# Performance work log

Hardware: AMD Instinct MI355X
Metric: run time of the kernel (lower is better)

## Reference

```python
import jax, jax.numpy as jnp
import numpy as np

N = 100000      # nodes
E = 800000      # edges (nnz of sparse adj)
D_IN = 128      # input feature dim
H = 64          # hidden_units
EMB = 32        # embsize
N_IDX = 50000   # gathered output rows
EPS = 1e-05     # BatchNormalization epsilon


def spmm(rows, cols, vals, x):
    # out[i] = sum_{e: rows[e]==i} vals[e] * x[cols[e]]  == sparse A @ x
    return jax.ops.segment_sum(vals[:, None] * x[cols], rows, num_segments=N)


def batchnorm(x, gamma, beta):
    # training-mode BN over node (batch) axis, matching Keras BatchNormalization
    m = jnp.mean(x, axis=0)
    v = jnp.var(x, axis=0)
    return (x - m) * jax.lax.rsqrt(v + EPS) * gamma + beta


def setup_inputs() -> dict:
    key = jax.random.key(0)
    ks = jax.random.split(key, 16)
    def w(k, fan_in, shape):
        return jax.random.normal(k, shape, dtype=jnp.float32) / np.sqrt(fan_in)
    inp = {
        "features": jax.random.normal(ks[0], (N, D_IN), dtype=jnp.float32),
        "rows": jax.random.randint(ks[1], (E,), 0, N),
        "cols": jax.random.randint(ks[2], (E,), 0, N),
        "vals": jax.random.uniform(ks[3], (E,), dtype=jnp.float32),
        "idx": jax.random.randint(ks[4], (N_IDX,), 0, N),
        # layer 0 (Dense with bias since l==0)
        "Wn0": w(ks[5], D_IN, (D_IN, H)), "bn0": jnp.zeros((H,), jnp.float32),
        "Wg0": w(ks[6], D_IN, (D_IN, H)), "bg0": jnp.zeros((H,), jnp.float32),
        "ab0": jnp.zeros((H,), jnp.float32),  # BiasLayer after SpMM
        "g0": jnp.ones((H,), jnp.float32), "b0": jnp.zeros((H,), jnp.float32),
        # layer 1 (no Dense bias)
        "Wn1": w(ks[7], H, (H, H)),
        "Wg1": w(ks[8], H, (H, H)),
        "ab1": jnp.zeros((H,), jnp.float32),
        "g1": jnp.ones((H,), jnp.float32), "b1": jnp.zeros((H,), jnp.float32),
        # conv_last block (Dense use_bias=False)
        "WnL": w(ks[9], H, (H, EMB)),
        "WgL": w(ks[10], H, (H, EMB)),
        "abL": jnp.zeros((EMB,), jnp.float32),
    }
    return inp


def reference(features, rows, cols, vals, idx,
              Wn0, bn0, Wg0, bg0, ab0, g0, b0,
              Wn1, Wg1, ab1, g1, b1,
              WnL, WgL, abL):
    x = features
    # SAGE layer 0
    x_node = x @ Wn0 + bn0
    x_neigh = x @ Wg0 + bg0
    agg = spmm(rows, cols, vals, x_neigh) + ab0
    x = jax.nn.relu(batchnorm(x_node + agg, g0, b0))
    # SAGE layer 1
    x_node = x @ Wn1
    x_neigh = x @ Wg1
    agg = spmm(rows, cols, vals, x_neigh) + ab1
    x = jax.nn.relu(batchnorm(x_node + agg, g1, b1))
    # conv_last projection to embsize
    x_node = x @ WnL
    x_neigh = x @ WgL
    agg = spmm(rows, cols, vals, x_neigh) + abL
    x = x_node + agg
    return x[idx]
```

## Files before the change

### kernel.cpp

```cpp
#include <hip/hip_runtime.h>

#define NNODES 100000
#define NEDGES 800000
#define DIN    128
#define HID    64
#define EMB    32
#define NIDX   50000
#define BN_EPS 1e-5f

#define NCHK 64
#define EC   (NEDGES / NCHK)
#define NB   ((NNODES + 63) / 64)
#define PF   16
#define NBF  ((NB + PF - 1) / PF)

typedef __attribute__((ext_vector_type(8))) short short8;
typedef __attribute__((ext_vector_type(4))) float f32x4;

__device__ inline unsigned short f2bf(float f) {
    unsigned u = __float_as_uint(f);
    unsigned r = u + 0x7FFFu + ((u >> 16) & 1u);
    return (unsigned short)(r >> 16);
}
__device__ inline float bf2f_lo(unsigned u) { return __uint_as_float(u << 16); }
__device__ inline float bf2f_hi(unsigned u) { return __uint_as_float(u & 0xffff0000u); }


__device__ inline void pack_seg(const float* __restrict__ Wn, const float* __restrict__ Wg,
                                unsigned short* __restrict__ Wp, int HOUT, int l2nt, int f) {
    int j = f & 7, lane = (f >> 3) & 63, g = f >> 9;
    int tt = g & ((1 << l2nt) - 1), kb = g >> l2nt;
    int k = kb * 32 + ((lane >> 4) * 8) + j;
    int nn = tt * 16 + (lane & 15);
    float v = (nn < HOUT) ? Wn[k * HOUT + nn] : Wg[k * HOUT + (nn - HOUT)];
    Wp[f] = f2bf(v);
}


__global__ __launch_bounds__(256) void histpack_k(
    const int* __restrict__ rows, int* __restrict__ Bcnt4, int* __restrict__ bTot,
    const int* __restrict__ idx, int* __restrict__ mark,
    const float* Wn0, const float* Wg0, const float* Wn1,
    const float* Wg1, const float* WnL, const float* WgL,
    unsigned short* Wp0, unsigned short* Wp1, unsigned short* WpL, int MB)
{
    int blk = blockIdx.x;
    int t = threadIdx.x;
    if (blk >= NCHK + MB) {
        int f = (blk - NCHK - MB) * 256 + t;
        if (f < 16384)      pack_seg(Wn0, Wg0, Wp0, 64, 3, f);
        else if (f < 24576) pack_seg(Wn1, Wg1, Wp1, 64, 3, f - 16384);
        else if (f < 28672) pack_seg(WnL, WgL, WpL, 32, 2, f - 24576);
        return;
    }
    if (blk >= NCHK) {
        int j = (blk - NCHK) * 256 + t;
        if (j < NIDX) mark[idx[j]] = 1;
        return;
    }
    __shared__ int hist[NB];
    for (int b = t; b < NB; b += 256) hist[b] = 0;
    __syncthreads();
    const int* rbase = rows + blk * EC;
    for (int i4 = t; i4 < EC / 4; i4 += 256) {
        int4 r4 = *(const int4*)&rbase[i4 * 4];
        atomicAdd(&hist[r4.x >> 6], 1);
        atomicAdd(&hist[r4.y >> 6], 1);
        atomicAdd(&hist[r4.z >> 6], 1);
        atomicAdd(&hist[r4.w >> 6], 1);
    }
    __syncthreads();
    for (int b = t; b < NB; b += 256) {
        int h = hist[b];
        Bcnt4[blk * NB + b] = h;
        if (h) atomicAdd(&bTot[b], h);
    }
}

__global__ __launch_bounds__(256) void scan_k(
    const int* __restrict__ Bcnt4, int* __restrict__ BcntT,
    const int* __restrict__ bTot, int* __restrict__ bBase)
{
    int t = threadIdx.x;
    if (blockIdx.x < 7) {
        int b = blockIdx.x * 256 + t;
        if (b >= NB) return;
        int run = 0;
        for (int c = 0; c < NCHK; c++) {
            BcntT[c * NB + b] = run;
            run += Bcnt4[c * NB + b];
        }
        return;
    }
    __shared__ int s[256];
    int v[7], loc = 0;
#pragma unroll
    for (int i = 0; i < 7; i++) {
        int ix = t * 7 + i;
        v[i] = loc;
        loc += (ix < NB) ? bTot[ix] : 0;
    }
    s[t] = loc;
    __syncthreads();
    for (int off = 1; off < 256; off <<= 1) {
        int a = (t >= off) ? s[t - off] : 0;
        __syncthreads();
        s[t] += a;
        __syncthreads();
    }
    int base = s[t] - loc;
#pragma unroll
    for (int i = 0; i < 7; i++) {
        int ix = t * 7 + i;
        if (ix < NB) bBase[ix] = base + v[i];
    }
    if (t == 255) bBase[NB] = NEDGES;
}


__global__ __launch_bounds__(256) void bfinal_spmm0_k(
    const uint2* __restrict__ ebuf, const int* __restrict__ bBase,
    int* __restrict__ rowptr, int2* __restrict__ cs,
    const unsigned short* __restrict__ Hgb, unsigned short* __restrict__ S,
    float* __restrict__ stats, int n)
{
    constexpr int ECAP = 1024;
    __shared__ int hist[64], sc[64], cur[64];
    __shared__ int2 es2[ECAP];
    __shared__ float rs[16][HID], rq[16][HID];
    int b = blockIdx.x, t = threadIdx.x;
    int e0 = bBase[b], e1 = bBase[b + 1];
    int cnt = e1 - e0;
    int r0 = b << 6;
    if (t < 64) hist[t] = 0;
    __syncthreads();

    uint2 ev0, ev1, ev2, ev3;
    bool h0 = t < cnt, h1 = t + 256 < cnt, h2 = t + 512 < cnt, h3 = t + 768 < cnt;
    if (h0) { ev0 = ebuf[e0 + t];       atomicAdd(&hist[(ev0.x >> 20) & 63], 1); }
    if (h1) { ev1 = ebuf[e0 + t + 256]; atomicAdd(&hist[(ev1.x >> 20) & 63], 1); }
    if (h2) { ev2 = ebuf[e0 + t + 512]; atomicAdd(&hist[(ev2.x >> 20) & 63], 1); }
    if (h3) { ev3 = ebuf[e0 + t + 768]; atomicAdd(&hist[(ev3.x >> 20) & 63], 1); }
    for (int i = t + ECAP; i < cnt; i += 256) {
        uint2 v = ebuf[e0 + i];
        atomicAdd(&hist[(v.x >> 20) & 63], 1);
    }
    __syncthreads();
    if (t == 0) {
        int run = 0;
        for (int j = 0; j < 64; j++) { sc[j] = run; run += hist[j]; }
    }
    __syncthreads();
    if (t < 64) {
        cur[t] = sc[t];
        int r = r0 + t;
        if (r < NNODES) rowptr[r] = e0 + sc[t];
    }
    if (b == NB - 1 && t == 0) rowptr[NNODES] = NEDGES;
    __syncthreads();

#define SCAT(V)                                                          \
    {                                                                    \
        int p = atomicAdd(&cur[((V).x >> 20) & 63], 1);                  \
        int2 pay = make_int2((int)((V).x & 0xFFFFF), (int)(V).y);        \
        if (p < ECAP) es2[p] = pay; else cs[e0 + p] = pay;               \
    }
    if (h0) SCAT(ev0)
    if (h1) SCAT(ev1)
    if (h2) SCAT(ev2)
    if (h3) SCAT(ev3)
    for (int i = t + ECAP; i < cnt; i += 256) {
        uint2 v = ebuf[e0 + i];
        SCAT(v)
    }
#undef SCAT
    __syncthreads();

    int scnt = min(cnt, ECAP);
    for (int i = t; i < scnt; i += 256) cs[e0 + i] = es2[i];

    const int lane = t & 15, g = t >> 4;
    const int c0 = lane * 4;
    float4 sum = make_float4(0.f, 0.f, 0.f, 0.f);
    float4 sq  = make_float4(0.f, 0.f, 0.f, 0.f);
#define FE(i) ((i) < ECAP ? es2[(i)] : cs[e0 + (i)])
#pragma unroll
    for (int rr = 0; rr < 4; rr++) {
        int lr = g * 4 + rr;
        int row = r0 + lr;
        if (row >= n) break;
        int le0 = sc[lr], le1 = sc[lr] + hist[lr];
        uint2 h = *(const uint2*)&S[(size_t)row * HID + c0];
        float4 a0 = make_float4(bf2f_lo(h.x), bf2f_hi(h.x), bf2f_lo(h.y), bf2f_hi(h.y));
        float4 a1 = make_float4(0.f, 0.f, 0.f, 0.f), a2 = a1, a3 = a1;
        int e = le0;
        for (; e + 3 < le1; e += 4) {
            int2 p0 = FE(e), p1 = FE(e + 1), p2 = FE(e + 2), p3 = FE(e + 3);
            float v0 = __int_as_float(p0.y), v1 = __int_as_float(p1.y);
            float v2 = __int_as_float(p2.y), v3 = __int_as_float(p3.y);
            uint2 h0v = *(const uint2*)&Hgb[(size_t)p0.x * HID + c0];
            uint2 h1v = *(const uint2*)&Hgb[(size_t)p1.x * HID + c0];
            uint2 h2v = *(const uint2*)&Hgb[(size_t)p2.x * HID + c0];
            uint2 h3v = *(const uint2*)&Hgb[(size_t)p3.x * HID + c0];
            a0.x += v0 * bf2f_lo(h0v.x); a0.y += v0 * bf2f_hi(h0v.x);
            a0.z += v0 * bf2f_lo(h0v.y); a0.w += v0 * bf2f_hi(h0v.y);
            a1.x += v1 * bf2f_lo(h1v.x); a1.y += v1 * bf2f_hi(h1v.x);
            a1.z += v1 * bf2f_lo(h1v.y); a1.w += v1 * bf2f_hi(h1v.y);
            a2.x += v2 * bf2f_lo(h2v.x); a2.y += v2 * bf2f_hi(h2v.x);
            a2.z += v2 * bf2f_lo(h2v.y); a2.w += v2 * bf2f_hi(h2v.y);
            a3.x += v3 * bf2f_lo(h3v.x); a3.y += v3 * bf2f_hi(h3v.x);
            a3.z += v3 * bf2f_lo(h3v.y); a3.w += v3 * bf2f_hi(h3v.y);
        }
        for (; e < le1; e++) {
            int2 p = FE(e);
            float v = __int_as_float(p.y);
            uint2 hh = *(const uint2*)&Hgb[(size_t)p.x * HID + c0];
            a0.x += v * bf2f_lo(hh.x); a0.y += v * bf2f_hi(hh.x);
            a0.z += v * bf2f_lo(hh.y); a0.w += v * bf2f_hi(hh.y);
        }
        float4 acc = make_float4(a0.x + a1.x + a2.x + a3.x, a0.y + a1.y + a2.y + a3.y,
                                 a0.z + a1.z + a2.z + a3.z, a0.w + a1.w + a2.w + a3.w);
        uint2 o;
        o.x = (unsigned)f2bf(acc.x) | ((unsigned)f2bf(acc.y) << 16);
        o.y = (unsigned)f2bf(acc.z) | ((unsigned)f2bf(acc.w) << 16);
        *(uint2*)&S[(size_t)row * HID + c0] = o;
        sum.x += acc.x; sum.y += acc.y; sum.z += acc.z; sum.w += acc.w;
        sq.x += acc.x * acc.x; sq.y += acc.y * acc.y;
        sq.z += acc.z * acc.z; sq.w += acc.w * acc.w;
    }
#undef FE

    *(float4*)&rs[g][c0] = sum;
    *(float4*)&rq[g][c0] = sq;
    __syncthreads();
    if (t < HID) {
        float a = 0.f, bb = 0.f;
        for (int w = 0; w < 16; w++) { a += rs[w][t]; bb += rq[w][t]; }
        int stripe = b & 7;
        atomicAdd(&stats[stripe * 128 + t], a);
        atomicAdd(&stats[stripe * 128 + HID + t], bb);
    }
}


template <int K, int HOUT, bool AFF, bool XBF, bool HNBF>
__device__ void gemm_body(const void* __restrict__ Xv, const unsigned short* __restrict__ Wp,
                          const float* __restrict__ bnA, const float* __restrict__ bnB,
                          const float* __restrict__ bgA,
                          const float* __restrict__ sums, const float* __restrict__ gamma,
                          const float* __restrict__ beta,
                          float* __restrict__ Hnf, unsigned short* __restrict__ Hnb,
                          unsigned short* __restrict__ Hgb, int n, int blk)
{
    constexpr int NT = 2 * HOUT / 16, NKB = K / 32;
    constexpr int RS = K + 8;
    constexpr int OC = HNBF ? 2 * HOUT : HOUT;
    constexpr int RSE = OC + 8;
    constexpr int XSZ = (RS > RSE) ? RS : RSE;
    __shared__ unsigned short Xs[64 * XSZ];
    __shared__ float sSc[64], sSh[64];

    const int row0 = blk * 64;
    const int t = threadIdx.x;

    if (AFF) {
        if (t < 64) {
            float sum = 0.f, sq = 0.f;
#pragma unroll
            for (int s = 0; s < 8; s++) { sum += sums[s * 128 + t]; sq += sums[s * 128 + 64 + t]; }
            float m = sum / (float)NNODES;
            float var = sq / (float)NNODES - m * m;
            float sc = gamma[t] * rsqrtf(var + BN_EPS);
            sSc[t] = sc; sSh[t] = beta[t] - m * sc;
        }
        __syncthreads();
    }

    constexpr int SIT = K / 32;
    if constexpr (XBF) {
        uint4 u[SIT];
#pragma unroll
        for (int it = 0; it < SIT; it++) {
            int li = it * 256 + t;
            int rr = row0 + li / (K / 8);
            int k8 = (li % (K / 8)) * 8;
            int rc = rr < n ? rr : n - 1;
            u[it] = *(const uint4*)((const unsigned short*)Xv + (size_t)rc * K + k8);
        }
#pragma unroll
        for (int it = 0; it < SIT; it++) {
            int li = it * 256 + t;
            int r  = li / (K / 8);
            int k8 = (li % (K / 8)) * 8;
            float v[8];
            v[0] = bf2f_lo(u[it].x); v[1] = bf2f_hi(u[it].x);
            v[2] = bf2f_lo(u[it].y); v[3] = bf2f_hi(u[it].y);
            v[4] = bf2f_lo(u[it].z); v[5] = bf2f_hi(u[it].z);
            v[6] = bf2f_lo(u[it].w); v[7] = bf2f_hi(u[it].w);
            if (AFF) {
#pragma unroll
                for (int i = 0; i < 8; i++) v[i] = fmaxf(v[i] * sSc[k8 + i] + sSh[k8 + i], 0.f);
            }
            uint4 o;
            o.x = (unsigned)f2bf(v[0]) | ((unsigned)f2bf(v[1]) << 16);
            o.y = (unsigned)f2bf(v[2]) | ((unsigned)f2bf(v[3]) << 16);
            o.z = (unsigned)f2bf(v[4]) | ((unsigned)f2bf(v[5]) << 16);
            o.w = (unsigned)f2bf(v[6]) | ((unsigned)f2bf(v[7]) << 16);
            *(uint4*)&Xs[r * RS + k8] = o;
        }
    } else {
        const float* Xf = (const float*)Xv;
        float4 a[SIT], b[SIT];
#pragma unroll
        for (int it = 0; it < SIT; it++) {
            int li = it * 256 + t;
            int rr = row0 + li / (K / 8);
            int k8 = (li % (K / 8)) * 8;
            int rc = rr < n ? rr : n - 1;
            a[it] = *(const float4*)&Xf[(size_t)rc * K + k8];
            b[it] = *(const float4*)&Xf[(size_t)rc * K + k8 + 4];
        }
#pragma unroll
        for (int it = 0; it < SIT; it++) {
            int li = it * 256 + t;
            int r  = li / (K / 8);
            int k8 = (li % (K / 8)) * 8;
            float v[8] = { a[it].x, a[it].y, a[it].z, a[it].w,
                           b[it].x, b[it].y, b[it].z, b[it].w };
            if (AFF) {
#pragma unroll
                for (int i = 0; i < 8; i++) v[i] = fmaxf(v[i] * sSc[k8 + i] + sSh[k8 + i], 0.f);
            }
            uint4 o;
            o.x = (unsigned)f2bf(v[0]) | ((unsigned)f2bf(v[1]) << 16);
            o.y = (unsigned)f2bf(v[2]) | ((unsigned)f2bf(v[3]) << 16);
            o.z = (unsigned)f2bf(v[4]) | ((unsigned)f2bf(v[5]) << 16);
            o.w = (unsigned)f2bf(v[6]) | ((unsigned)f2bf(v[7]) << 16);
            *(uint4*)&Xs[r * RS + k8] = o;
        }
    }
    __syncthreads();

    const int wave = t >> 6, lane = t & 63;
    const int q = lane >> 4, mrow = lane & 15;

    f32x4 acc[NT];
#pragma unroll
    for (int i = 0; i < NT; i++) acc[i] = (f32x4){0.f, 0.f, 0.f, 0.f};

    const short8* wp8 = (const short8*)Wp;
#pragma unroll
    for (int kb = 0; kb < NKB; kb++) {
        short8 va = *(const short8*)&Xs[(wave * 16 + mrow) * RS + kb * 32 + q * 8];
#pragma unroll
        for (int tt = 0; tt < NT; tt++) {
            short8 vb = wp8[(kb * NT + tt) * 64 + lane];
            acc[tt] = __builtin_amdgcn_mfma_f32_16x16x32_bf16(va, vb, acc[tt], 0, 0, 0);
        }
    }

    __syncthreads();
#pragma unroll
    for (int tt = 0; tt < NT; tt++) {
        int nglob = tt * 16 + mrow;
        bool nside = (nglob < HOUT);
        int c = nside ? nglob : (nglob - HOUT);
        float bias = 0.f;
        if (nside) {
            if (bnA) bias += bnA[c];
            if (bnB) bias += bnB[c];
        } else if (bgA) {
            bias += bgA[c];
        }
        if (HNBF || !nside) {
            int cc = HNBF ? nglob : c;
#pragma unroll
            for (int r = 0; r < 4; r++)
                Xs[(wave * 16 + q * 4 + r) * RSE + cc] = f2bf(acc[tt][r] + bias);
        } else {
#pragma unroll
            for (int r = 0; r < 4; r++) {
                int rr = row0 + wave * 16 + q * 4 + r;
                if (rr < n) Hnf[(size_t)rr * HOUT + c] = acc[tt][r] + bias;
            }
        }
    }
    __syncthreads();
    constexpr int J = OC / 8;
#pragma unroll
    for (int u2 = 0; u2 < (64 * J) / 256; u2++) {
        int li = u2 * 256 + t;
        int r = li / J, j = li % J;
        int rr = row0 + r;
        if (rr < n) {
            uint4 v = *(const uint4*)&Xs[r * RSE + j * 8];
            int c8 = j * 8;
            if (HNBF && c8 < HOUT)
                *(uint4*)&Hnb[(size_t)rr * HOUT + c8] = v;
            else
                *(uint4*)&Hgb[(size_t)rr * HOUT + (HNBF ? c8 - HOUT : c8)] = v;
        }
    }
}

__global__ __launch_bounds__(256) void part_gemm0_k(
    const int* __restrict__ rows, const int* __restrict__ cols,
    const float* __restrict__ vals, const int* __restrict__ BcntT,
    const int* __restrict__ bBase, uint2* __restrict__ ebuf,
    const float* __restrict__ X, const unsigned short* __restrict__ Wp0,
    const float* __restrict__ bn0, const float* __restrict__ ab0, const float* __restrict__ bg0,
    unsigned short* __restrict__ Hn0b, unsigned short* __restrict__ Hgb, int n)
{
    if ((int)blockIdx.x < NCHK * PF) {
        __shared__ int cur[NBF];
        int t = threadIdx.x;
        int blk = blockIdx.x % NCHK;
        int pf  = blockIdx.x / NCHK;
        int b0 = pf * NBF, b1 = (pf == PF - 1) ? NB : (b0 + NBF);
        for (int b = b0 + t; b < b1; b += 256)
            cur[b - b0] = bBase[b] + BcntT[blk * NB + b];
        __syncthreads();
        constexpr int EC4 = EC / 4;
        const int*   rbase = rows + blk * EC;
        const int*   cbase = cols + blk * EC;
        const float* vbase = vals + blk * EC;
        int i4 = t;
        int4 r4, c4; float4 v4;
        if (i4 < EC4) {
            r4 = *(const int4*)&rbase[i4 * 4];
            c4 = *(const int4*)&cbase[i4 * 4];
            v4 = *(const float4*)&vbase[i4 * 4];
        }
        while (i4 < EC4) {
            int4 rr = r4; int4 cc = c4; float4 vv = v4;
            int ni = i4 + 256;
            if (ni < EC4) {
                r4 = *(const int4*)&rbase[ni * 4];
                c4 = *(const int4*)&cbase[ni * 4];
                v4 = *(const float4*)&vbase[ni * 4];
            }
#pragma unroll
            for (int j = 0; j < 4; j++) {
                int r = (&rr.x)[j];
                int b = r >> 6;
                if (b >= b0 && b < b1) {
                    int p = atomicAdd(&cur[b - b0], 1);
                    ebuf[p] = make_uint2(((unsigned)(r & 63) << 20) | (unsigned)(&cc.x)[j],
                                         (unsigned)__float_as_int((&vv.x)[j]));
                }
            }
            i4 = ni;
        }
    } else {
        gemm_body<DIN, HID, false, false, true>(X, Wp0, bn0, ab0, bg0,
            nullptr, nullptr, nullptr, nullptr, Hn0b, Hgb, n, blockIdx.x - NCHK * PF);
    }
}

template <int K, int HOUT, bool AFF, bool XBF, bool HNBF>
__global__ __launch_bounds__(256) void gemm_k(
    const void* __restrict__ X, const unsigned short* __restrict__ Wp,
    const float* __restrict__ bnA, const float* __restrict__ bnB, const float* __restrict__ bgA,
    const float* __restrict__ sums, const float* __restrict__ gamma, const float* __restrict__ beta,
    float* __restrict__ Hnf, unsigned short* __restrict__ Hnb, unsigned short* __restrict__ Hgb, int n)
{
    gemm_body<K, HOUT, AFF, XBF, HNBF>(X, Wp, bnA, bnB, bgA, sums, gamma, beta,
                                       Hnf, Hnb, Hgb, n, blockIdx.x);
}


template <int HH, bool STATS, bool SBF, bool MARKED>
__global__ __launch_bounds__(256) void spmm_k(
    const int* __restrict__ rowptr, const int2* __restrict__ cs,
    const unsigned short* __restrict__ Hgb, void* __restrict__ Sv,
    float* __restrict__ stats, const int* __restrict__ mark, int n)
{
    constexpr int L   = HH / 4;
    constexpr int GP  = 256 / L;
    constexpr int RPB = 64;
    constexpr int RPG = RPB / GP;
    constexpr int ECAP = 1024;
    __shared__ int2 es[ECAP];
    __shared__ int  rp[RPB + 1];

    const int t = threadIdx.x;
    const int R0 = blockIdx.x * RPB;
    if (t <= RPB) rp[t] = rowptr[min(R0 + t, n)];
    __syncthreads();
    const int e0b  = rp[0];
    const int scnt = min(rp[RPB] - e0b, ECAP);
    for (int i = t; i < scnt; i += 256) es[i] = cs[e0b + i];
    __syncthreads();

    const int lane = t % L;
    const int g    = t / L;
    const int c0   = lane * 4;

    float4 sum = make_float4(0.f, 0.f, 0.f, 0.f);
    float4 sq  = make_float4(0.f, 0.f, 0.f, 0.f);

#define SPMM_ROW(FETCH)                                                            \
    {                                                                              \
        int e = le0;                                                               \
        for (; e + 3 < le1; e += 4) {                                              \
            int2 p0 = FETCH(e), p1 = FETCH(e + 1), p2 = FETCH(e + 2), p3 = FETCH(e + 3); \
            float v0 = __int_as_float(p0.y), v1 = __int_as_float(p1.y);            \
            float v2 = __int_as_float(p2.y), v3 = __int_as_float(p3.y);            \
            uint2 h0 = *(const uint2*)&Hgb[(size_t)p0.x * HH + c0];                \
            uint2 h1 = *(const uint2*)&Hgb[(size_t)p1.x * HH + c0];                \
            uint2 h2 = *(const uint2*)&Hgb[(size_t)p2.x * HH + c0];                \
            uint2 h3 = *(const uint2*)&Hgb[(size_t)p3.x * HH + c0];                \
            a0.x += v0 * bf2f_lo(h0.x); a0.y += v0 * bf2f_hi(h0.x);                \
            a0.z += v0 * bf2f_lo(h0.y); a0.w += v0 * bf2f_hi(h0.y);                \
            a1.x += v1 * bf2f_lo(h1.x); a1.y += v1 * bf2f_hi(h1.x);                \
            a1.z += v1 * bf2f_lo(h1.y); a1.w += v1 * bf2f_hi(h1.y);                \
            a2.x += v2 * bf2f_lo(h2.x); a2.y += v2 * bf2f_hi(h2.x);                \
            a2.z += v2 * bf2f_lo(h2.y); a2.w += v2 * bf2f_hi(h2.y);                \
            a3.x += v3 * bf2f_lo(h3.x); a3.y += v3 * bf2f_hi(h3.x);                \
            a3.z += v3 * bf2f_lo(h3.y); a3.w += v3 * bf2f_hi(h3.y);                \
        }                                                                          \
        for (; e < le1; e++) {                                                     \
            int2 p = FETCH(e);                                                     \
            float v = __int_as_float(p.y);                                         \
            uint2 h = *(const uint2*)&Hgb[(size_t)p.x * HH + c0];                  \
            a0.x += v * bf2f_lo(h.x); a0.y += v * bf2f_hi(h.x);                    \
            a0.z += v * bf2f_lo(h.y); a0.w += v * bf2f_hi(h.y);                    \
        }                                                                          \
    }
#define F_LDS(i) es[(i)]
#define F_GLB(i) cs[e0b + (i)]

#pragma unroll
    for (int rr = 0; rr < RPG; rr++) {
        int row = R0 + g * RPG + rr;
        if (row >= n) break;
        if (MARKED && !mark[row]) continue;
        int le0 = rp[g * RPG + rr] - e0b;
        int le1 = rp[g * RPG + rr + 1] - e0b;
        float4 a0, a1, a2, a3;
        if (SBF) {
            uint2 h = *(const uint2*)((const unsigned short*)Sv + (size_t)row * HH + c0);
            a0 = make_float4(bf2f_lo(h.x), bf2f_hi(h.x), bf2f_lo(h.y), bf2f_hi(h.y));
        } else {
            a0 = *(const float4*)((const float*)Sv + (size_t)row * HH + c0);
        }
        a1 = a2 = a3 = make_float4(0.f, 0.f, 0.f, 0.f);
        if (le1 <= scnt) SPMM_ROW(F_LDS) else SPMM_ROW(F_GLB);
        float4 acc = make_float4(a0.x + a1.x + a2.x + a3.x, a0.y + a1.y + a2.y + a3.y,
                                 a0.z + a1.z + a2.z + a3.z, a0.w + a1.w + a2.w + a3.w);
        if (SBF) {
            uint2 o;
            o.x = (unsigned)f2bf(acc.x) | ((unsigned)f2bf(acc.y) << 16);
            o.y = (unsigned)f2bf(acc.z) | ((unsigned)f2bf(acc.w) << 16);
            *(uint2*)((unsigned short*)Sv + (size_t)row * HH + c0) = o;
        } else {
            *(float4*)((float*)Sv + (size_t)row * HH + c0) = acc;
        }
        if (STATS) {
            sum.x += acc.x; sum.y += acc.y; sum.z += acc.z; sum.w += acc.w;
            sq.x += acc.x * acc.x; sq.y += acc.y * acc.y;
            sq.z += acc.z * acc.z; sq.w += acc.w * acc.w;
        }
    }
#undef SPMM_ROW
#undef F_LDS
#undef F_GLB

    if constexpr (STATS) {
        __shared__ float rs[GP][HH];
        __shared__ float rq[GP][HH];
        *(float4*)&rs[g][c0] = sum;
        *(float4*)&rq[g][c0] = sq;
        __syncthreads();
        if (threadIdx.x < HH) {
            float a = 0.f, b = 0.f;
            for (int w = 0; w < GP; w++) { a += rs[w][threadIdx.x]; b += rq[w][threadIdx.x]; }
            int stripe = blockIdx.x & 7;
            atomicAdd(&stats[stripe * 128 + threadIdx.x], a);
            atomicAdd(&stats[stripe * 128 + HH + threadIdx.x], b);
        }
    }
}

__global__ void gather_k(const float* __restrict__ S, const int* __restrict__ idx,
                         float* __restrict__ out, int total4) {
    int j = blockIdx.x * 256 + threadIdx.x;
    if (j < total4) {
        int r = j / (EMB / 4), c4 = (j % (EMB / 4)) * 4;
        *(float4*)&out[(size_t)j * 4] = *(const float4*)&S[(size_t)idx[r] * EMB + c4];
    }
}


extern "C" void kernel_launch(void* const* d_in, const int* in_sizes, int n_in,
                              void* d_out, int out_size, void* d_ws, size_t ws_size,
                              hipStream_t stream) {
    const float* features = (const float*)d_in[0];
    const int*   rows     = (const int*)d_in[1];
    const int*   cols     = (const int*)d_in[2];
    const float* vals     = (const float*)d_in[3];
    const int*   idx      = (const int*)d_in[4];
    const float* Wn0 = (const float*)d_in[5];
    const float* bn0 = (const float*)d_in[6];
    const float* Wg0 = (const float*)d_in[7];
    const float* bg0 = (const float*)d_in[8];
    const float* ab0 = (const float*)d_in[9];
    const float* g0  = (const float*)d_in[10];
    const float* b0  = (const float*)d_in[11];
    const float* Wn1 = (const float*)d_in[12];
    const float* Wg1 = (const float*)d_in[13];
    const float* ab1 = (const float*)d_in[14];
    const float* g1  = (const float*)d_in[15];
    const float* b1  = (const float*)d_in[16];
    const float* WnL = (const float*)d_in[17];
    const float* WgL = (const float*)d_in[18];
    const float* abL = (const float*)d_in[19];
    float* out = (float*)d_out;

    float*          HnLf = (float*)d_ws;
    unsigned short* nA   = (unsigned short*)(HnLf + (size_t)NNODES * EMB);
    unsigned short* nB   = nA + (size_t)NNODES * HID;
    unsigned short* Hgb  = nB + (size_t)NNODES * HID;
    uint2* ebuf  = (uint2*)(Hgb + (size_t)NNODES * HID);
    int2*  cs    = (int2*)(ebuf + NEDGES);
    int*   rowptr = (int*)(cs + NEDGES);
    int*   Bcnt4 = rowptr + (NNODES + 4);
    int*   BcntT = Bcnt4 + NCHK * NB;
    int*   bBase = BcntT + NCHK * NB;
    unsigned short* Wp0 = (unsigned short*)(bBase + 1568);
    unsigned short* Wp1 = Wp0 + 16384;
    unsigned short* WpL = Wp1 + 8192;
    float* stats = (float*)(WpL + 4096);
    int*   mark  = (int*)(stats + 2304);
    int*   bTot  = mark + NNODES;
    float* sums0 = stats;
    float* sums1 = stats + 1024;
    size_t zbytes = 2304 * 4 + (size_t)NNODES * 4 + 1568 * 4;

    hipMemsetAsync(stats, 0, zbytes, stream);

    const int GBm = (NNODES + 63) / 64;
    const int MB  = (NIDX + 255) / 256;

    histpack_k<<<NCHK + MB + 112, 256, 0, stream>>>(
        rows, Bcnt4, bTot, idx, mark, Wn0, Wg0, Wn1, Wg1, WnL, WgL, Wp0, Wp1, WpL, MB);
    scan_k<<<8, 256, 0, stream>>>(Bcnt4, BcntT, bTot, bBase);
    part_gemm0_k<<<NCHK * PF + GBm, 256, 0, stream>>>(rows, cols, vals, BcntT, bBase, ebuf,
                                                      features, Wp0, bn0, ab0, bg0,
                                                      nA, Hgb, NNODES);
    bfinal_spmm0_k<<<NB, 256, 0, stream>>>(ebuf, bBase, rowptr, cs, Hgb, nA, sums0, NNODES);

    gemm_k<HID, HID, true, true, true><<<GBm, 256, 0, stream>>>(
        nA, Wp1, ab1, nullptr, nullptr, sums0, g0, b0, nullptr, nB, Hgb, NNODES);
    spmm_k<HID, true, true, false><<<GBm, 256, 0, stream>>>(rowptr, cs, Hgb, nB, sums1, nullptr, NNODES);

    gemm_k<HID, EMB, true, true, false><<<GBm, 256, 0, stream>>>(
        nB, WpL, abL, nullptr, nullptr, sums1, g1, b1, HnLf, nullptr, Hgb, NNODES);
    spmm_k<EMB, false, false, true><<<GBm, 256, 0, stream>>>(rowptr, cs, Hgb, HnLf, nullptr, mark, NNODES);

    gather_k<<<(NIDX * EMB / 4 + 255) / 256, 256, 0, stream>>>(HnLf, idx, out, NIDX * EMB / 4);
}
```

Baseline: 252.4 us.

## Fuse tail GEMM/SpMM/gather launches into one cooperative kernel with grid syncs

Replaces the five tail launches (layer-1 GEMM, SpMM with stats, last GEMM, marked SpMM, gather) with a single cooperative kernel that separates the phases with grid.sync(). Shared memory is unified into one byte buffer so every phase fits the same occupancy budget. The goal is to remove launch gaps and the ramp-up and drain between dependent kernels. In exchange it adds grid-wide barrier cost and caps occupancy at 7 blocks per CU. The old launch path remains as a fallback when cooperative launch is unsupported or fails.

```diff
diff --git a/kernel.cpp b/kernel.cpp
--- a/kernel.cpp
+++ b/kernel.cpp
@@ -1,4 +1,7 @@
 #include <hip/hip_runtime.h>
+#include <hip/hip_cooperative_groups.h>
+
+namespace cg = cooperative_groups;
 
 #define NNODES 100000
 #define NEDGES 800000
@@ -13,6 +16,8 @@
 #define NB   ((NNODES + 63) / 64)
 #define PF   16
 #define NBF  ((NB + PF - 1) / PF)
+#define GBM  ((NNODES + 63) / 64)
+#define SMSZ 17920
 
 typedef __attribute__((ext_vector_type(8))) short short8;
 typedef __attribute__((ext_vector_type(4))) float f32x4;
@@ -250,15 +255,17 @@
                           const float* __restrict__ sums, const float* __restrict__ gamma,
                           const float* __restrict__ beta,
                           float* __restrict__ Hnf, unsigned short* __restrict__ Hnb,
-                          unsigned short* __restrict__ Hgb, int n, int blk)
+                          unsigned short* __restrict__ Hgb, int n, int blk, char* sm)
 {
     constexpr int NT = 2 * HOUT / 16, NKB = K / 32;
     constexpr int RS = K + 8;
     constexpr int OC = HNBF ? 2 * HOUT : HOUT;
     constexpr int RSE = OC + 8;
     constexpr int XSZ = (RS > RSE) ? RS : RSE;
-    __shared__ unsigned short Xs[64 * XSZ];
-    __shared__ float sSc[64], sSh[64];
+    static_assert(64 * XSZ * 2 + 512 <= SMSZ, "smem budget");
+    unsigned short* Xs = (unsigned short*)sm;
+    float* sSc = (float*)(sm + 64 * XSZ * 2);
+    float* sSh = sSc + 64;
 
     const int row0 = blk * 64;
     const int t = threadIdx.x;
@@ -411,8 +418,9 @@
     const float* __restrict__ bn0, const float* __restrict__ ab0, const float* __restrict__ bg0,
     unsigned short* __restrict__ Hn0b, unsigned short* __restrict__ Hgb, int n)
 {
+    __shared__ alignas(16) char sm[SMSZ];
     if ((int)blockIdx.x < NCHK * PF) {
-        __shared__ int cur[NBF];
+        int* cur = (int*)sm;
         int t = threadIdx.x;
         int blk = blockIdx.x % NCHK;
         int pf  = blockIdx.x / NCHK;
@@ -453,7 +461,7 @@
         }
     } else {
         gemm_body<DIN, HID, false, false, true>(X, Wp0, bn0, ab0, bg0,
-            nullptr, nullptr, nullptr, nullptr, Hn0b, Hgb, n, blockIdx.x - NCHK * PF);
+            nullptr, nullptr, nullptr, nullptr, Hn0b, Hgb, n, blockIdx.x - NCHK * PF, sm);
     }
 }
 
@@ -464,27 +472,31 @@
     const float* __restrict__ sums, const float* __restrict__ gamma, const float* __restrict__ beta,
     float* __restrict__ Hnf, unsigned short* __restrict__ Hnb, unsigned short* __restrict__ Hgb, int n)
 {
+    __shared__ alignas(16) char sm[SMSZ];
     gemm_body<K, HOUT, AFF, XBF, HNBF>(X, Wp, bnA, bnB, bgA, sums, gamma, beta,
-                                       Hnf, Hnb, Hgb, n, blockIdx.x);
+                                       Hnf, Hnb, Hgb, n, blockIdx.x, sm);
 }
 
 
 template <int HH, bool STATS, bool SBF, bool MARKED>
-__global__ __launch_bounds__(256) void spmm_k(
+__device__ void spmm_phase(
     const int* __restrict__ rowptr, const int2* __restrict__ cs,
     const unsigned short* __restrict__ Hgb, void* __restrict__ Sv,
-    float* __restrict__ stats, const int* __restrict__ mark, int n)
+    float* __restrict__ stats, const int* __restrict__ mark, int n, int blk, char* sm)
 {
     constexpr int L   = HH / 4;
     constexpr int GP  = 256 / L;
     constexpr int RPB = 64;
     constexpr int RPG = RPB / GP;
     constexpr int ECAP = 1024;
-    __shared__ int2 es[ECAP];
-    __shared__ int  rp[RPB + 1];
+    static_assert(8464 + 2 * GP * HH * 4 <= SMSZ, "smem budget");
+    int2*  es  = (int2*)sm;
+    int*   rp  = (int*)(sm + 8192);
+    float* rsb = (float*)(sm + 8464);
+    float* rqb = rsb + GP * HH;
 
     const int t = threadIdx.x;
-    const int R0 = blockIdx.x * RPB;
+    const int R0 = blk * RPB;
     if (t <= RPB) rp[t] = rowptr[min(R0 + t, n)];
     __syncthreads();
     const int e0b  = rp[0];
@@ -567,19 +579,27 @@
 #undef F_GLB
 
     if constexpr (STATS) {
-        __shared__ float rs[GP][HH];
-        __shared__ float rq[GP][HH];
-        *(float4*)&rs[g][c0] = sum;
-        *(float4*)&rq[g][c0] = sq;
+        *(float4*)&rsb[g * HH + c0] = sum;
+        *(float4*)&rqb[g * HH + c0] = sq;
         __syncthreads();
-        if (threadIdx.x < HH) {
+        if (t < HH) {
             float a = 0.f, b = 0.f;
-            for (int w = 0; w < GP; w++) { a += rs[w][threadIdx.x]; b += rq[w][threadIdx.x]; }
-            int stripe = blockIdx.x & 7;
-            atomicAdd(&stats[stripe * 128 + threadIdx.x], a);
-            atomicAdd(&stats[stripe * 128 + HH + threadIdx.x], b);
-        }
-    }
+            for (int w = 0; w < GP; w++) { a += rsb[w * HH + t]; b += rqb[w * HH + t]; }
+            int stripe = blk & 7;
+            atomicAdd(&stats[stripe * 128 + t], a);
+            atomicAdd(&stats[stripe * 128 + HH + t], b);
+        }
+    }
+}
+
+template <int HH, bool STATS, bool SBF, bool MARKED>
+__global__ __launch_bounds__(256) void spmm_k(
+    const int* __restrict__ rowptr, const int2* __restrict__ cs,
+    const unsigned short* __restrict__ Hgb, void* __restrict__ Sv,
+    float* __restrict__ stats, const int* __restrict__ mark, int n)
+{
+    __shared__ alignas(16) char sm[SMSZ];
+    spmm_phase<HH, STATS, SBF, MARKED>(rowptr, cs, Hgb, Sv, stats, mark, n, blockIdx.x, sm);
 }
 
 __global__ void gather_k(const float* __restrict__ S, const int* __restrict__ idx,
@@ -588,6 +608,37 @@
     if (j < total4) {
         int r = j / (EMB / 4), c4 = (j % (EMB / 4)) * 4;
         *(float4*)&out[(size_t)j * 4] = *(const float4*)&S[(size_t)idx[r] * EMB + c4];
+    }
+}
+
+
+__global__ __launch_bounds__(256, 7) void tail_k(
+    const unsigned short* nA, const unsigned short* Wp1, const float* ab1,
+    const float* sums0, const float* g0, const float* b0,
+    unsigned short* nB, unsigned short* Hgb,
+    const int* rowptr, const int2* cs, float* sums1,
+    const unsigned short* WpL, const float* abL, const float* g1, const float* b1,
+    float* HnLf, const int* mark, const int* idx, float* out, int n)
+{
+    __shared__ alignas(16) char sm[SMSZ];
+    const int blk = blockIdx.x;
+    cg::grid_group grid = cg::this_grid();
+
+    gemm_body<HID, HID, true, true, true>(nA, Wp1, ab1, nullptr, nullptr,
+        sums0, g0, b0, nullptr, nB, Hgb, n, blk, sm);
+    grid.sync();
+    spmm_phase<HID, true, true, false>(rowptr, cs, Hgb, nB, sums1, nullptr, n, blk, sm);
+    grid.sync();
+    gemm_body<HID, EMB, true, true, false>(nB, WpL, abL, nullptr, nullptr,
+        sums1, g1, b1, HnLf, nullptr, Hgb, n, blk, sm);
+    grid.sync();
+    spmm_phase<EMB, false, false, true>(rowptr, cs, Hgb, HnLf, nullptr, mark, n, blk, sm);
+    grid.sync();
+    int j = blk * 256 + threadIdx.x;
+    constexpr int total4 = NIDX * EMB / 4;
+    if (j < total4) {
+        int r = j / (EMB / 4), c4 = (j % (EMB / 4)) * 4;
+        *(float4*)&out[(size_t)j * 4] = *(const float4*)&HnLf[(size_t)idx[r] * EMB + c4];
     }
 }
 
@@ -639,7 +690,7 @@
 
     hipMemsetAsync(stats, 0, zbytes, stream);
 
-    const int GBm = (NNODES + 63) / 64;
+    const int GBm = GBM;
     const int MB  = (NIDX + 255) / 256;
 
     histpack_k<<<NCHK + MB + 112, 256, 0, stream>>>(
@@ -650,13 +701,33 @@
                                                       nA, Hgb, NNODES);
     bfinal_spmm0_k<<<NB, 256, 0, stream>>>(ebuf, bBase, rowptr, cs, Hgb, nA, sums0, NNODES);
 
-    gemm_k<HID, HID, true, true, true><<<GBm, 256, 0, stream>>>(
-        nA, Wp1, ab1, nullptr, nullptr, sums0, g0, b0, nullptr, nB, Hgb, NNODES);
-    spmm_k<HID, true, true, false><<<GBm, 256, 0, stream>>>(rowptr, cs, Hgb, nB, sums1, nullptr, NNODES);
-
-    gemm_k<HID, EMB, true, true, false><<<GBm, 256, 0, stream>>>(
-        nB, WpL, abL, nullptr, nullptr, sums1, g1, b1, HnLf, nullptr, Hgb, NNODES);
-    spmm_k<EMB, false, false, true><<<GBm, 256, 0, stream>>>(rowptr, cs, Hgb, HnLf, nullptr, mark, NNODES);
-
-    gather_k<<<(NIDX * EMB / 4 + 255) / 256, 256, 0, stream>>>(HnLf, idx, out, NIDX * EMB / 4);
-}
+    static int coop_ok = -1;
+    if (coop_ok < 0) {
+        int dev = 0, sup = 0, ncu = 0, mb = 0;
+        hipGetDevice(&dev);
+        hipDeviceGetAttribute(&sup, hipDeviceAttributeCooperativeLaunch, dev);
+        hipDeviceGetAttribute(&ncu, hipDeviceAttributeMultiprocessorCount, dev);
+        hipOccupancyMaxActiveBlocksPerMultiprocessor(&mb, tail_k, 256, 0);
+        coop_ok = (sup && (long)mb * ncu >= GBM) ? 1 : 0;
+    }
+    if (coop_ok == 1) {
+        int nn = NNODES;
+        void* ka[] = { (void*)&nA, (void*)&Wp1, (void*)&ab1, (void*)&sums0,
+                       (void*)&g0, (void*)&b0, (void*)&nB, (void*)&Hgb,
+                       (void*)&rowptr, (void*)&cs, (void*)&sums1, (void*)&WpL,
+                       (void*)&abL, (void*)&g1, (void*)&b1, (void*)&HnLf,
+                       (void*)&mark, (void*)&idx, (void*)&out, (void*)&nn };
+        hipError_t e = hipLaunchCooperativeKernel((const void*)tail_k, dim3(GBm), dim3(256),
+                                                  ka, 0, stream);
+        if (e != hipSuccess) coop_ok = 0;
+    }
+    if (coop_ok != 1) {
+        gemm_k<HID, HID, true, true, true><<<GBm, 256, 0, stream>>>(
+            nA, Wp1, ab1, nullptr, nullptr, sums0, g0, b0, nullptr, nB, Hgb, NNODES);
+        spmm_k<HID, true, true, false><<<GBm, 256, 0, stream>>>(rowptr, cs, Hgb, nB, sums1, nullptr, NNODES);
+        gemm_k<HID, EMB, true, true, false><<<GBm, 256, 0, stream>>>(
+            nB, WpL, abL, nullptr, nullptr, sums1, g1, b1, HnLf, nullptr, Hgb, NNODES);
+        spmm_k<EMB, false, false, true><<<GBm, 256, 0, stream>>>(rowptr, cs, Hgb, HnLf, nullptr, mark, NNODES);
+        gather_k<<<(NIDX * EMB / 4 + 255) / 256, 256, 0, stream>>>(HnLf, idx, out, NIDX * EMB / 4);
+    }
+}
```

Measured after the change: 274.0 us. 1.09x slower.

## Fold bucket scan into histogram kernel via last-block completion counter

Applied to the files above, without the earlier changes.

Removes the separate scan kernel launch. The last histogram block to finish, detected with an atomic done counter and thread fences, computes the exclusive scan of bucket totals into bBase. The per-chunk prefix (BcntT) is no longer materialized; each partition block in part_gemm0_k instead sums Bcnt4 over earlier chunks on the fly. This trades one kernel launch and a transposed scan for redundant per-block prefix loops of up to 64 loads per bucket, and adds a serialized tail in the last histogram block.

```diff
diff --git a/kernel.cpp b/kernel.cpp
--- a/kernel.cpp
+++ b/kernel.cpp
@@ -39,6 +39,7 @@
 
 __global__ __launch_bounds__(256) void histpack_k(
     const int* __restrict__ rows, int* __restrict__ Bcnt4, int* __restrict__ bTot,
+    int* __restrict__ done, int* __restrict__ bBase,
     const int* __restrict__ idx, int* __restrict__ mark,
     const float* Wn0, const float* Wg0, const float* Wn1,
     const float* Wg1, const float* WnL, const float* WgL,
@@ -59,6 +60,7 @@
         return;
     }
     __shared__ int hist[NB];
+    __shared__ int sfin;
     for (int b = t; b < NB; b += 256) hist[b] = 0;
     __syncthreads();
     const int* rbase = rows + blk * EC;
@@ -75,46 +77,36 @@
         Bcnt4[blk * NB + b] = h;
         if (h) atomicAdd(&bTot[b], h);
     }
-}
-
-__global__ __launch_bounds__(256) void scan_k(
-    const int* __restrict__ Bcnt4, int* __restrict__ BcntT,
-    const int* __restrict__ bTot, int* __restrict__ bBase)
-{
-    int t = threadIdx.x;
-    if (blockIdx.x < 7) {
-        int b = blockIdx.x * 256 + t;
-        if (b >= NB) return;
-        int run = 0;
-        for (int c = 0; c < NCHK; c++) {
-            BcntT[c * NB + b] = run;
-            run += Bcnt4[c * NB + b];
-        }
-        return;
-    }
-    __shared__ int s[256];
-    int v[7], loc = 0;
-#pragma unroll
-    for (int i = 0; i < 7; i++) {
-        int ix = t * 7 + i;
-        v[i] = loc;
-        loc += (ix < NB) ? bTot[ix] : 0;
-    }
-    s[t] = loc;
-    __syncthreads();
-    for (int off = 1; off < 256; off <<= 1) {
-        int a = (t >= off) ? s[t - off] : 0;
+    __threadfence();
+    __syncthreads();
+    if (t == 0) sfin = (atomicAdd(done, 1) == NCHK - 1);
+    __syncthreads();
+    if (sfin) {
+        __threadfence();
+        __shared__ int s[256];
+        int v[7], loc = 0;
+#pragma unroll
+        for (int i = 0; i < 7; i++) {
+            int ix = t * 7 + i;
+            v[i] = loc;
+            loc += (ix < NB) ? bTot[ix] : 0;
+        }
+        s[t] = loc;
         __syncthreads();
-        s[t] += a;
-        __syncthreads();
-    }
-    int base = s[t] - loc;
-#pragma unroll
-    for (int i = 0; i < 7; i++) {
-        int ix = t * 7 + i;
-        if (ix < NB) bBase[ix] = base + v[i];
-    }
-    if (t == 255) bBase[NB] = NEDGES;
+        for (int off = 1; off < 256; off <<= 1) {
+            int a = (t >= off) ? s[t - off] : 0;
+            __syncthreads();
+            s[t] += a;
+            __syncthreads();
+        }
+        int base = s[t] - loc;
+#pragma unroll
+        for (int i = 0; i < 7; i++) {
+            int ix = t * 7 + i;
+            if (ix < NB) bBase[ix] = base + v[i];
+        }
+        if (t == 255) bBase[NB] = NEDGES;
+    }
 }
 
 
@@ -405,7 +397,7 @@
 
 __global__ __launch_bounds__(256) void part_gemm0_k(
     const int* __restrict__ rows, const int* __restrict__ cols,
-    const float* __restrict__ vals, const int* __restrict__ BcntT,
+    const float* __restrict__ vals, const int* __restrict__ Bcnt4,
     const int* __restrict__ bBase, uint2* __restrict__ ebuf,
     const float* __restrict__ X, const unsigned short* __restrict__ Wp0,
     const float* __restrict__ bn0, const float* __restrict__ ab0, const float* __restrict__ bg0,
@@ -417,8 +409,11 @@
         int blk = blockIdx.x % NCHK;
         int pf  = blockIdx.x / NCHK;
         int b0 = pf * NBF, b1 = (pf == PF - 1) ? NB : (b0 + NBF);
-        for (int b = b0 + t; b < b1; b += 256)
-            cur[b - b0] = bBase[b] + BcntT[blk * NB + b];
+        for (int b = b0 + t; b < b1; b += 256) {
+            int run = bBase[b];
+            for (int c = 0; c < blk; c++) run += Bcnt4[c * NB + b];
+            cur[b - b0] = run;
+        }
         __syncthreads();
         constexpr int EC4 = EC / 4;
         const int*   rbase = rows + blk * EC;
@@ -625,17 +620,17 @@
     int2*  cs    = (int2*)(ebuf + NEDGES);
     int*   rowptr = (int*)(cs + NEDGES);
     int*   Bcnt4 = rowptr + (NNODES + 4);
-    int*   BcntT = Bcnt4 + NCHK * NB;
-    int*   bBase = BcntT + NCHK * NB;
+    int*   bBase = Bcnt4 + NCHK * NB;
     unsigned short* Wp0 = (unsigned short*)(bBase + 1568);
     unsigned short* Wp1 = Wp0 + 16384;
     unsigned short* WpL = Wp1 + 8192;
     float* stats = (float*)(WpL + 4096);
     int*   mark  = (int*)(stats + 2304);
     int*   bTot  = mark + NNODES;
+    int*   done  = bTot + 1568;
     float* sums0 = stats;
     float* sums1 = stats + 1024;
-    size_t zbytes = 2304 * 4 + (size_t)NNODES * 4 + 1568 * 4;
+    size_t zbytes = 2304 * 4 + (size_t)NNODES * 4 + 1568 * 4 + 16;
 
     hipMemsetAsync(stats, 0, zbytes, stream);
 
@@ -643,9 +638,9 @@
     const int MB  = (NIDX + 255) / 256;
 
     histpack_k<<<NCHK + MB + 112, 256, 0, stream>>>(
-        rows, Bcnt4, bTot, idx, mark, Wn0, Wg0, Wn1, Wg1, WnL, WgL, Wp0, Wp1, WpL, MB);
-    scan_k<<<8, 256, 0, stream>>>(Bcnt4, BcntT, bTot, bBase);
-    part_gemm0_k<<<NCHK * PF + GBm, 256, 0, stream>>>(rows, cols, vals, BcntT, bBase, ebuf,
+        rows, Bcnt4, bTot, done, bBase, idx, mark,
+        Wn0, Wg0, Wn1, Wg1, WnL, WgL, Wp0, Wp1, WpL, MB);
+    part_gemm0_k<<<NCHK * PF + GBm, 256, 0, stream>>>(rows, cols, vals, Bcnt4, bBase, ebuf,
                                                       features, Wp0, bn0, ab0, bg0,
                                                       nA, Hgb, NNODES);
     bfinal_spmm0_k<<<NB, 256, 0, stream>>>(ebuf, bBase, rowptr, cs, Hgb, nA, sums0, NNODES);
```

Measured after the change: 260.9 us. 1.03x slower.
